# Kernel tuning notes

Hardware: AMD Instinct MI355X
Metric: run time of the kernel (lower is better)

The kernel has to match this reference:

```python
import jax, jax.numpy as jnp
import numpy as np

B, O, H, I = 256, 128, 1024, 2048  # batch, objects, hidden, input_size
Hh = H // 2  # 512; x_j feature dim
DF = I - Hh  # 1536; X_F feature dim


def _xavier(key, shape):
    fan_in, fan_out = shape[1], shape[0]
    lim = np.sqrt(6.0 / (fan_in + fan_out))
    return jax.random.uniform(key, shape, jnp.float32, -lim, lim)


def setup_inputs() -> dict:
    key = jax.random.key(0)
    ks = jax.random.split(key, 24)
    mask = jax.random.bernoulli(ks[0], 0.7, (B, O))
    mask = mask.at[:, 0].set(True)  # ensure at least one valid object per row
    inp = {
        "x_j": jax.random.normal(ks[1], (B, O, Hh), jnp.float32),
        "x_mask": mask,
        "X_F": jax.random.normal(ks[2], (B, DF), jnp.float32),
        "h": jax.random.normal(ks[3], (B, 1, H), jnp.float32),
        "c": jax.random.normal(ks[4], (B, 1, H), jnp.float32),
    }
    names_W = ["W_i", "W_f", "W_c", "W_o"]
    names_U = ["U_i", "U_f", "U_c", "U_o"]
    names_V = ["V_i", "V_f", "V_c", "V_o"]
    k = 5
    for n in names_W:
        inp[n] = _xavier(ks[k], (H, I)); k += 1
    for n in names_U + names_V:
        inp[n] = _xavier(ks[k], (H, H)); k += 1
    for n in ["b_i", "b_f", "b_c", "b_o"]:
        inp[n] = jnp.zeros((H,), jnp.float32)
    inp["w"] = _xavier(ks[k], (1, Hh)); k += 1
    inp["W_e"] = _xavier(ks[k], (Hh, H)); k += 1
    inp["U_e"] = _xavier(ks[k], (Hh, Hh)); k += 1
    inp["b_e"] = jnp.zeros((Hh,), jnp.float32)
    return inp


def reference(x_j, x_mask, X_F, h, c,
              W_i, W_f, W_c, W_o,
              U_i, U_f, U_c, U_o,
              V_i, V_f, V_c, V_o,
              b_i, b_f, b_c, b_o,
              w, W_e, U_e, b_e):
    # Additive attention over objects.
    # h: (B,1,H) -> (B,1,Hh) broadcasts against x_j proj (B,O,Hh)
    e = jnp.tanh(h @ W_e.T + x_j @ U_e.T + b_e)      # (B,O,Hh)
    e = (e @ w.T)[..., 0]                              # (B,O)
    e = jnp.where(x_mask, e, -1e9)
    a = jax.nn.softmax(e, axis=1)                      # (B,O)
    phi_j = jnp.einsum('bo,bok->bk', a, x_j)[:, None, :]  # (B,1,Hh)
    x = jnp.concatenate([phi_j, X_F[:, None, :]], axis=2)  # (B,1,I)

    # Peephole LSTM gates (h, c: (B,1,H))
    i = jax.nn.sigmoid(x @ W_i.T + h @ U_i.T + c @ V_i.T + b_i)
    f = jax.nn.sigmoid(x @ W_f.T + h @ U_f.T + c @ V_f.T + b_f)
    new_c = f * c + i * jnp.tanh(x @ W_c.T + h @ U_c.T + b_c)
    o = jax.nn.sigmoid(x @ W_o.T + h @ U_o.T + c @ V_o.T + b_o)
    new_h = o * jnp.tanh(new_c)
    return new_h, new_c
```

## Files before the change

kernel.cpp:

```cpp
#include <hip/hip_runtime.h>
#include <hip/hip_bf16.h>

typedef unsigned char u8;
typedef unsigned short u16;
typedef unsigned int u32;
typedef __attribute__((ext_vector_type(8))) short bf8;
typedef __attribute__((ext_vector_type(4))) float f4;

#define B_ 256
#define O_ 128
#define Hh_ 512
#define H_ 1024
#define DF_ 1536
#define I_ 2048

#define HWE_OFF   0
#define XC_OFF    524288
#define PRE_OFF   2621440
#define FLAG_OFF  6815744
#define XJ16_OFF  7340032
#define UE16_OFF  40894464
#define WS_BIG    41418752
#define GPART_OFF XJ16_OFF

__device__ __forceinline__ float bf1(u16 u){ union{u32 i; float f;} v; v.i = ((u32)u)<<16; return v.f; }
__device__ __forceinline__ u16 f2bf(float f){
    __hip_bfloat16 h = __float2bfloat16(f);
    union{ __hip_bfloat16 h; u16 u; } v; v.h = h; return v.u;
}
__device__ __forceinline__ u32 pack2(float a, float b){
    return ((u32)f2bf(a)) | (((u32)f2bf(b))<<16);
}
struct P8 { uint4 lo, hi; };
__device__ __forceinline__ P8 fetch8(const void* p, size_t idx, int isf32){
    P8 r;
    if(isf32){
        const uint4* f = (const uint4*)((const float*)p + idx);
        r.lo = f[0]; r.hi = f[1];
    } else {
        r.lo = *(const uint4*)((const u16*)p + idx);
    }
    return r;
}
__device__ __forceinline__ uint4 cvt8(P8 r, int isf32){
    if(isf32){
        float4 x = *(float4*)&r.lo, y = *(float4*)&r.hi;
        uint4 o;
        o.x = pack2(x.x,x.y); o.y = pack2(x.z,x.w);
        o.z = pack2(y.x,y.y); o.w = pack2(y.z,y.w);
        return o;
    }
    return r.lo;
}
__device__ __forceinline__ uint4 load8(const void* p, size_t idx, int isf32){
    return cvt8(fetch8(p, idx, isf32), isf32);
}
__device__ __forceinline__ float loads(const void* p, size_t idx, int isf32){
    return isf32 ? ((const float*)p)[idx] : bf1(((const u16*)p)[idx]);
}
__device__ __forceinline__ float fast_tanh(float x){
    return 1.0f - 2.0f/(__expf(2.0f*x)+1.0f);
}
__device__ __forceinline__ float sigmoidf_(float x){
    return 1.0f/(1.0f+__expf(-x));
}

__global__ void k_detect(const u8* __restrict__ m, const u16* __restrict__ xj,
                         int* __restrict__ flags){
    __shared__ int n1, n2, n3, mb, xo;
    int t = threadIdx.x;
    if(t==0){ n1=0; n2=0; n3=0; mb=0; xo=0; }
    __syncthreads();
    int a1=0, a2=0, a3=0, amax=0;
    for(int i=t; i<8192; i+=256){
        int v = m[i]; int c = i&3;
        if(c==1) a1|=v;
        if(c==2) a2|=v;
        if(c==3) a3|=v;
        amax = amax > v ? amax : v;
    }
    if(a1) atomicOr(&n1,1);
    if(a2) atomicOr(&n2,1);
    if(a3) atomicOr(&n3,1);
    atomicMax(&mb, amax);
    int e = 0;
    for(int i=t; i<2048; i+=256){
        u32 u = xj[2*i];
        int ex = (u>>7)&0xFF;
        if(ex >= 156) e = 1;
    }
    if(e) atomicOr(&xo,1);
    __syncthreads();
    if(t==0){
        int w;
        if(!n1 && !n2 && !n3)      w = 4;
        else if(!n1 && n2 && n3)   w = 4;
        else if(mb > 1)            w = 2;
        else                       w = 1;
        flags[0] = w;
        flags[1] = xo;
    }
}

__global__ __launch_bounds__(256) void k_pack(const void* __restrict__ XF,
                                              const void* __restrict__ h,
                                              const void* __restrict__ c,
                                              const void* __restrict__ Ue,
                                              const int* __restrict__ flags,
                                              int packN,
                                              u16* __restrict__ Xc,
                                              u16* __restrict__ ue16){
    int bid = blockIdx.x, t = threadIdx.x;
    int isf32 = flags[1];
    if(bid < packN){
        int b = bid/14;
        int r = (bid%14)*256 + t;
        float v;
        if(r < DF_)            v = loads(XF, (size_t)b*DF_ + r, isf32);
        else if(r < DF_ + H_)  v = loads(h,  (size_t)b*H_ + (r - DF_), isf32);
        else                   v = loads(c,  (size_t)b*H_ + (r - DF_ - H_), isf32);
        Xc[(size_t)b*4096 + 512 + r] = f2bf(v);
    } else {
        size_t g = (size_t)(bid - packN)*256 + t;
        size_t idx = g*8;
        *(uint4*)&ue16[idx] = load8(Ue, idx, isf32);
    }
}

__global__ __launch_bounds__(256) void k_hwe(const void* __restrict__ h,
                                             const void* __restrict__ We,
                                             const int* __restrict__ flags,
                                             float* __restrict__ hwe){
    int n0 = blockIdx.x*64;
    int kc = blockIdx.y*128;
    int m0 = blockIdx.z*128;
    int t = threadIdx.x;
    int isf32 = flags[1];
    __shared__ __align__(16) u16 As[128*40];
    __shared__ __align__(16) u16 Bs[64*40];
    int w = t>>6, lane = t&63;
    int q = lane>>4, l16 = lane&15;
    int koff = q*8;
    f4 acc[2][4];
    for(int mi=0;mi<2;mi++) for(int ni=0;ni<4;ni++){
        f4 z = {0.f,0.f,0.f,0.f}; acc[mi][ni] = z;
    }
    for(int ks=0; ks<128; ks+=32){
        __syncthreads();
        for(int i=0;i<2;i++){
            int row = i*64 + (t>>2), cv = t&3;
            uint4 va = load8(h, (size_t)(m0+row)*H_ + kc + ks + cv*8, isf32);
            *(uint4*)&As[row*40 + cv*8] = va;
        }
        {
            int row = t>>2, cv = t&3;
            uint4 vb = load8(We, (size_t)(n0+row)*H_ + kc + ks + cv*8, isf32);
            *(uint4*)&Bs[row*40 + cv*8] = vb;
        }
        __syncthreads();
        bf8 af[2], bfr[4];
        for(int mi=0;mi<2;mi++) af[mi]  = *(const bf8*)&As[(w*32+mi*16+l16)*40 + koff];
        for(int ni=0;ni<4;ni++) bfr[ni] = *(const bf8*)&Bs[(ni*16+l16)*40 + koff];
        for(int mi=0;mi<2;mi++)
            for(int ni=0;ni<4;ni++)
                acc[mi][ni] = __builtin_amdgcn_mfma_f32_16x16x32_bf16(af[mi], bfr[ni], acc[mi][ni], 0,0,0);
    }
    for(int mi=0;mi<2;mi++){
        for(int r=0;r<4;r++){
            int brow = m0 + w*32 + mi*16 + q*4 + r;
            for(int ni=0;ni<4;ni++){
                int ncol = n0 + ni*16 + l16;
                atomicAdd(&hwe[(size_t)brow*Hh_ + ncol], acc[mi][ni][r]);
            }
        }
    }
}

__global__ __launch_bounds__(512) void k_attn(const void* __restrict__ xjA,
                                              const void* __restrict__ wvec,
                                              const void* __restrict__ UeA,
                                              const void* __restrict__ be,
                                              const float* __restrict__ hwe,
                                              const int* __restrict__ flags,
                                              int srcbfB,
                                              float* __restrict__ Epart){
    int b = blockIdx.x, y = blockIdx.y, t = threadIdx.x;
    int isf = flags[1];
    int isA = isf;
    int isB = srcbfB ? 0 : isf;
    __shared__ __align__(16) u16 As[128*40];
    __shared__ __align__(16) u16 Bs[128*40];
    __shared__ float hwes[128];
    __shared__ float wvs[128];

    if(t < 128){
        int col = y*128 + t;
        hwes[t] = hwe[(size_t)b*Hh_ + col] + loads(be, col, isf);
        wvs[t]  = loads(wvec, col, isf);
    }

    const size_t xboff = (size_t)b*O_*Hh_;
    int w = t>>6, lane = t&63;
    int q = lane>>4, l16 = lane&15;
    int koff = q*8;
    int rA = t>>2, cA = t&3;

    f4 acc[8];
    for(int ni=0;ni<8;ni++){
        f4 z = {0.f,0.f,0.f,0.f}; acc[ni] = z;
    }

    P8 pa, pb;
    pa = fetch8(xjA, xboff + (size_t)rA*Hh_        + cA*8, isA);
    pb = fetch8(UeA, (size_t)(y*128 + rA)*Hh_      + cA*8, isB);

    for(int ks=0; ks<Hh_; ks+=32){
        __syncthreads();
        *(uint4*)&As[rA*40 + cA*8] = cvt8(pa, isA);
        *(uint4*)&Bs[rA*40 + cA*8] = cvt8(pb, isB);
        __syncthreads();
        if(ks + 32 < Hh_){
            int kn = ks + 32;
            pa = fetch8(xjA, xboff + (size_t)rA*Hh_        + kn + cA*8, isA);
            pb = fetch8(UeA, (size_t)(y*128 + rA)*Hh_      + kn + cA*8, isB);
        }
        bf8 af, bfr[8];
        af = *(const bf8*)&As[(w*16+l16)*40 + koff];
        for(int ni=0;ni<8;ni++) bfr[ni] = *(const bf8*)&Bs[(ni*16+l16)*40 + koff];
        for(int ni=0;ni<8;ni++)
            acc[ni] = __builtin_amdgcn_mfma_f32_16x16x32_bf16(af, bfr[ni], acc[ni], 0,0,0);
    }
    for(int r=0;r<4;r++){
        int o = w*16 + q*4 + r;
        float part = 0.f;
        for(int ni=0;ni<8;ni++){
            int col = ni*16 + l16;
            part += wvs[col] * fast_tanh(hwes[col] + acc[ni][r]);
        }
        part += __shfl_xor(part, 1);
        part += __shfl_xor(part, 2);
        part += __shfl_xor(part, 4);
        part += __shfl_xor(part, 8);
        if(l16 == 0) Epart[(size_t)y*32768 + (size_t)b*O_ + o] = part;
    }
}

__global__ __launch_bounds__(512) void k_soft(const float* __restrict__ Epart,
                                              const void* __restrict__ maskp,
                                              const void* __restrict__ xjA,
                                              const int* __restrict__ flags,
                                              u16* __restrict__ Xc){
    int b = blockIdx.x, t = threadIdx.x;
    int isf = flags[1];
    int isA = isf;
    int mw = flags[0];
    __shared__ float es[O_];
    __shared__ float as_[O_];
    __shared__ float red[2];
    if(t < O_){
        float e = 0.f;
        for(int p=0;p<4;p++) e += Epart[(size_t)p*32768 + (size_t)b*O_ + t];
        size_t mi_ = (size_t)b*O_ + t;
        bool valid;
        if(mw == 1)      valid = ((const u8*)maskp)[mi_]  != 0;
        else if(mw == 2) valid = ((const u16*)maskp)[mi_] != 0;
        else             valid = ((const u32*)maskp)[mi_] != 0;
        es[t] = valid ? e : -1e30f;
    }
    __syncthreads();
    if(t < 64){
        float v = fmaxf(es[t], es[t+64]);
        for(int m=32;m>0;m>>=1) v = fmaxf(v, __shfl_xor(v, m));
        if(t==0) red[0] = v;
    }
    __syncthreads();
    if(t < O_) as_[t] = __expf(es[t] - red[0]);
    __syncthreads();
    if(t < 64){
        float v = as_[t] + as_[t+64];
        for(int m=32;m>0;m>>=1) v += __shfl_xor(v, m);
        if(t==0) red[1] = v;
    }
    __syncthreads();
    float inv = 1.0f / red[1];
    float acc = 0.f;
    size_t base = (size_t)b*O_*Hh_ + t;
    #pragma unroll 8
    for(int o=0;o<O_;o++){
        acc += as_[o] * loads(xjA, base + (size_t)o*Hh_, isA);
    }
    Xc[(size_t)b*4096 + t] = f2bf(acc * inv);
}

__global__ __launch_bounds__(512) void k_gates(const u16* __restrict__ Xc,
    const void* __restrict__ Wi, const void* __restrict__ Wf, const void* __restrict__ Wc, const void* __restrict__ Wo,
    const void* __restrict__ Ui, const void* __restrict__ Uf, const void* __restrict__ Uc, const void* __restrict__ Uo,
    const void* __restrict__ Vi, const void* __restrict__ Vf, const void* __restrict__ Vo,
    const int* __restrict__ flags,
    int dosplit,
    float* __restrict__ part){
    int nt = blockIdx.x;
    int kc = blockIdx.y;
    int g  = nt>>4;
    int k0 = kc*512;
    if(g == 2 && k0 >= 3072) return;
    int isf32 = flags[1];
    const void* Wm = (g==0)?Wi:(g==1)?Wf:(g==2)?Wc:Wo;
    const void* Um = (g==0)?Ui:(g==1)?Uf:(g==2)?Uc:Uo;
    const void* Vm = (g==0)?Vi:(g==1)?Vf:(g==3)?Vo:Vi;
    int n0 = (nt&15)*64;
    int t = threadIdx.x;
    __shared__ __align__(16) u16 As[256*40];
    __shared__ __align__(16) u16 Bs[64*40];
    int w = t>>6, lane = t&63;
    int q = lane>>4, l16 = lane&15;
    int koff = q*8;
    int rA = t>>2, cA = t&3;
    bool hasB = (t < 256);

    f4 acc[2][4];
    for(int mi=0;mi<2;mi++) for(int ni=0;ni<4;ni++){
        f4 z = {0.f,0.f,0.f,0.f}; acc[mi][ni] = z;
    }

    auto fetchB = [&](int k)->P8{
        int n = n0 + rA;
        if(k < 2048)       return fetch8(Wm, (size_t)n*I_ + k, isf32);
        else if(k < 3072)  return fetch8(Um, (size_t)n*H_ + (k-2048), isf32);
        else               return fetch8(Vm, (size_t)n*H_ + (k-3072), isf32);
    };

    uint4 qa0, qa1; P8 qb;
    qa0 = *(const uint4*)(Xc + (size_t)rA*4096       + k0 + cA*8);
    qa1 = *(const uint4*)(Xc + (size_t)(rA+128)*4096 + k0 + cA*8);
    if(hasB) qb = fetchB(k0 + cA*8);

    for(int ks=0; ks<512; ks+=32){
        __syncthreads();
        *(uint4*)&As[rA*40 + cA*8]       = qa0;
        *(uint4*)&As[(rA+128)*40 + cA*8] = qa1;
        if(hasB) *(uint4*)&Bs[rA*40 + cA*8] = cvt8(qb, isf32);
        __syncthreads();
        if(ks + 32 < 512){
            int kn = k0 + ks + 32;
            qa0 = *(const uint4*)(Xc + (size_t)rA*4096       + kn + cA*8);
            qa1 = *(const uint4*)(Xc + (size_t)(rA+128)*4096 + kn + cA*8);
            if(hasB) qb = fetchB(kn + cA*8);
        }
        bf8 af[2], bfr[4];
        for(int mi=0;mi<2;mi++) af[mi]  = *(const bf8*)&As[(w*32+mi*16+l16)*40 + koff];
        for(int ni=0;ni<4;ni++) bfr[ni] = *(const bf8*)&Bs[(ni*16+l16)*40 + koff];
        for(int mi=0;mi<2;mi++)
            for(int ni=0;ni<4;ni++)
                acc[mi][ni] = __builtin_amdgcn_mfma_f32_16x16x32_bf16(af[mi], bfr[ni], acc[mi][ni], 0,0,0);
    }
    float* pg = dosplit ? (part + ((size_t)kc*4 + g)*(size_t)(B_*H_))
                        : (part + (size_t)g*(B_*H_));
    for(int mi=0;mi<2;mi++){
        for(int r=0;r<4;r++){
            int brow = w*32 + mi*16 + q*4 + r;
            for(int ni=0;ni<4;ni++){
                int ncol = n0 + ni*16 + l16;
                size_t o = (size_t)brow*H_ + ncol;
                if(dosplit) pg[o] = acc[mi][ni][r];
                else        atomicAdd(&pg[o], acc[mi][ni][r]);
            }
        }
    }
}

__global__ __launch_bounds__(256) void k_combine(const float* __restrict__ part,
    int nsplit, int climit,
    const void* __restrict__ c,
    const void* __restrict__ bi, const void* __restrict__ bfv,
    const void* __restrict__ bc, const void* __restrict__ bo,
    const int* __restrict__ flags,
    float* __restrict__ out){
    int b = blockIdx.x, t = threadIdx.x;
    int isf32 = flags[1];
    const size_t G = (size_t)B_*H_;
    for(int i=0;i<4;i++){
        int n = i*256 + t;
        size_t idx = (size_t)b*H_ + n;
        float pi = 0.f, pf = 0.f, pcv = 0.f, po = 0.f;
        for(int p=0;p<nsplit;p++){
            const float* pp = part + (size_t)p*4*G;
            pi += pp[idx];
            pf += pp[G + idx];
            po += pp[3*G + idx];
            if(p < climit) pcv += pp[2*G + idx];
        }
        pi  += loads(bi,  n, isf32);
        pf  += loads(bfv, n, isf32);
        pcv += loads(bc,  n, isf32);
        po  += loads(bo,  n, isf32);
        float ig = sigmoidf_(pi);
        float fg = sigmoidf_(pf);
        float og = sigmoidf_(po);
        float cold = loads(c, idx, isf32);
        float ncv = fg*cold + ig*fast_tanh(pcv);
        float nh  = og*fast_tanh(ncv);
        out[idx]     = nh;
        out[G + idx] = ncv;
    }
}

extern "C" void kernel_launch(void* const* d_in, const int* in_sizes, int n_in,
                              void* d_out, int out_size, void* d_ws, size_t ws_size,
                              hipStream_t stream){
    const void* xj   = d_in[0];
    const void* mask = d_in[1];
    const void* XF   = d_in[2];
    const void* h    = d_in[3];
    const void* c    = d_in[4];
    const void* Wi   = d_in[5];
    const void* Wf   = d_in[6];
    const void* Wc   = d_in[7];
    const void* Wo   = d_in[8];
    const void* Ui   = d_in[9];
    const void* Uf   = d_in[10];
    const void* Uc   = d_in[11];
    const void* Uo   = d_in[12];
    const void* Vi   = d_in[13];
    const void* Vf   = d_in[14];
    const void* Vo   = d_in[16];
    const void* bi   = d_in[17];
    const void* bfv  = d_in[18];
    const void* bc   = d_in[19];
    const void* bo   = d_in[20];
    const void* wv   = d_in[21];
    const void* We   = d_in[22];
    const void* Ue   = d_in[23];
    const void* be   = d_in[24];

    char* ws = (char*)d_ws;
    float* hwe  = (float*)(ws + HWE_OFF);
    u16*   Xc   = (u16*)(ws + XC_OFF);
    float* pre  = (float*)(ws + PRE_OFF);
    int*   flags= (int*)(ws + FLAG_OFF);
    float* out  = (float*)d_out;

    int big = (ws_size >= (size_t)WS_BIG);
    u16* ue16 = (u16*)(ws + UE16_OFF);
    float* gpart = (float*)(ws + GPART_OFF);
    const void* UeA = big ? (const void*)ue16 : Ue;

    k_detect<<<1, 256, 0, stream>>>((const u8*)mask, (const u16*)xj, flags);
    hipMemsetAsync(hwe, 0, (size_t)B_*Hh_*sizeof(float), stream);
    k_pack<<<3584 + (big ? 256 : 0), 256, 0, stream>>>(XF, h, c, Ue, flags, 3584, Xc, ue16);
    k_hwe<<<dim3(8,8,2), 256, 0, stream>>>(h, We, flags, hwe);
    k_attn<<<dim3(B_, 4), 512, 0, stream>>>(xj, wv, UeA, be, hwe, flags, big, pre);
    k_soft<<<B_, 512, 0, stream>>>(pre, mask, xj, flags, Xc);
    if(big){
        k_gates<<<dim3(64, 8), 512, 0, stream>>>(Xc, Wi,Wf,Wc,Wo, Ui,Uf,Uc,Uo, Vi,Vf,Vo, flags, 1, gpart);
        k_combine<<<B_, 256, 0, stream>>>(gpart, 8, 6, c, bi, bfv, bc, bo, flags, out);
    } else {
        hipMemsetAsync(pre, 0, (size_t)4*B_*H_*sizeof(float), stream);
        k_gates<<<dim3(64, 8), 512, 0, stream>>>(Xc, Wi,Wf,Wc,Wo, Ui,Uf,Uc,Uo, Vi,Vf,Vo, flags, 0, pre);
        k_combine<<<B_, 256, 0, stream>>>(pre, 1, 1, c, bi, bfv, bc, bo, flags, out);
    }
}
```

Baseline: 297.7 us.

## Fuse detect, pack and hwe GEMM into one prep kernel and drop memset

Removes the single-block detect kernel and its flags buffer; each kernel now works out the dtype and mask-width flags itself with a wave ballot on a few elements. The Ue conversion, the h·We^T GEMM and the X packing are merged into one launch, and the hwe memset plus atomics are replaced by four split-K partial buffers that k_attn sums. This cuts three launches and the serial detect step, at the cost of redundant detection reads in every block and a heuristic that samples fewer elements. hweP sits inside the PRE region, which the attention partials also use, so overlap is a risk.

```diff
diff --git a/kernel.cpp b/kernel.cpp
--- a/kernel.cpp
+++ b/kernel.cpp
@@ -14,10 +14,9 @@
 #define DF_ 1536
 #define I_ 2048
 
-#define HWE_OFF   0
 #define XC_OFF    524288
 #define PRE_OFF   2621440
-#define FLAG_OFF  6815744
+#define HWEP_OFF  (PRE_OFF + 1048576)
 #define XJ16_OFF  7340032
 #define UE16_OFF  40894464
 #define WS_BIG    41418752
@@ -65,54 +64,99 @@
     return 1.0f/(1.0f+__expf(-x));
 }
 
-__global__ void k_detect(const u8* __restrict__ m, const u16* __restrict__ xj,
-                         int* __restrict__ flags){
-    __shared__ int n1, n2, n3, mb, xo;
-    int t = threadIdx.x;
-    if(t==0){ n1=0; n2=0; n3=0; mb=0; xo=0; }
-    __syncthreads();
-    int a1=0, a2=0, a3=0, amax=0;
-    for(int i=t; i<8192; i+=256){
-        int v = m[i]; int c = i&3;
-        if(c==1) a1|=v;
-        if(c==2) a2|=v;
-        if(c==3) a3|=v;
-        amax = amax > v ? amax : v;
-    }
-    if(a1) atomicOr(&n1,1);
-    if(a2) atomicOr(&n2,1);
-    if(a3) atomicOr(&n3,1);
-    atomicMax(&mb, amax);
-    int e = 0;
-    for(int i=t; i<2048; i+=256){
-        u32 u = xj[2*i];
-        int ex = (u>>7)&0xFF;
-        if(ex >= 156) e = 1;
-    }
-    if(e) atomicOr(&xo,1);
-    __syncthreads();
-    if(t==0){
-        int w;
-        if(!n1 && !n2 && !n3)      w = 4;
-        else if(!n1 && n2 && n3)   w = 4;
-        else if(mb > 1)            w = 2;
-        else                       w = 1;
-        flags[0] = w;
-        flags[1] = xo;
-    }
-}
-
-__global__ __launch_bounds__(256) void k_pack(const void* __restrict__ XF,
+__device__ __forceinline__ int detect_isf32(const void* xj){
+    int l = threadIdx.x & 63;
+    u32 u = ((const u16*)xj)[2*l];
+    int ex = (u>>7)&0xFF;
+    unsigned long long m = __ballot(ex >= 156);
+    return m != 0ULL;
+}
+__device__ __forceinline__ int detect_mw(const void* maskp){
+    int l = threadIdx.x & 63;
+    u32 v = ((const u32*)maskp)[l];
+    int b0 =  v      & 0xFF;
+    int b1 = (v>>8)  & 0xFF;
+    int b2 = (v>>16) & 0xFF;
+    int b3 = (v>>24) & 0xFF;
+    unsigned long long n1 = __ballot(b1 != 0);
+    unsigned long long n2 = __ballot(b2 != 0);
+    unsigned long long n3 = __ballot(b3 != 0);
+    int mx = max(max(b0,b1), max(b2,b3));
+    for(int s=32;s>0;s>>=1) mx = max(mx, __shfl_xor(mx, s));
+    int w;
+    if(!n1 && !n2 && !n3)      w = 4;
+    else if(!n1 && n2 && n3)   w = 4;
+    else if(mx > 1)            w = 2;
+    else                       w = 1;
+    return w;
+}
+
+__global__ __launch_bounds__(256) void k_prep(const void* __restrict__ xj,
+                                              const void* __restrict__ Ue,
+                                              const void* __restrict__ XF,
                                               const void* __restrict__ h,
                                               const void* __restrict__ c,
-                                              const void* __restrict__ Ue,
-                                              const int* __restrict__ flags,
-                                              int packN,
-                                              u16* __restrict__ Xc,
-                                              u16* __restrict__ ue16){
+                                              const void* __restrict__ We,
+                                              int ueN,
+                                              u16* __restrict__ ue16,
+                                              float* __restrict__ hweP,
+                                              u16* __restrict__ Xc){
     int bid = blockIdx.x, t = threadIdx.x;
-    int isf32 = flags[1];
-    if(bid < packN){
+    int isf32 = detect_isf32(xj);
+    if(bid < ueN){
+        size_t g = (size_t)bid*256 + t;
+        size_t idx = g*8;
+        *(uint4*)&ue16[idx] = load8(Ue, idx, isf32);
+        return;
+    }
+    bid -= ueN;
+    if(bid < 64){
+        int n0 = (bid&7)*64;
+        int kb = ((bid>>3)&3)*256;
+        int m0 = (bid>>5)*128;
+        __shared__ __align__(16) u16 As[128*40];
+        __shared__ __align__(16) u16 Bs[64*40];
+        int w = t>>6, lane = t&63;
+        int q = lane>>4, l16 = lane&15;
+        int koff = q*8;
+        f4 acc[2][4];
+        for(int mi=0;mi<2;mi++) for(int ni=0;ni<4;ni++){
+            f4 z = {0.f,0.f,0.f,0.f}; acc[mi][ni] = z;
+        }
+        for(int ks=0; ks<256; ks+=32){
+            __syncthreads();
+            for(int i=0;i<2;i++){
+                int row = i*64 + (t>>2), cv = t&3;
+                uint4 va = load8(h, (size_t)(m0+row)*H_ + kb + ks + cv*8, isf32);
+                *(uint4*)&As[row*40 + cv*8] = va;
+            }
+            {
+                int row = t>>2, cv = t&3;
+                uint4 vb = load8(We, (size_t)(n0+row)*H_ + kb + ks + cv*8, isf32);
+                *(uint4*)&Bs[row*40 + cv*8] = vb;
+            }
+            __syncthreads();
+            bf8 af[2], bfr[4];
+            for(int mi=0;mi<2;mi++) af[mi]  = *(const bf8*)&As[(w*32+mi*16+l16)*40 + koff];
+            for(int ni=0;ni<4;ni++) bfr[ni] = *(const bf8*)&Bs[(ni*16+l16)*40 + koff];
+            for(int mi=0;mi<2;mi++)
+                for(int ni=0;ni<4;ni++)
+                    acc[mi][ni] = __builtin_amdgcn_mfma_f32_16x16x32_bf16(af[mi], bfr[ni], acc[mi][ni], 0,0,0);
+        }
+        float* hp = hweP + (size_t)((bid>>3)&3)*(B_*Hh_);
+        for(int mi=0;mi<2;mi++){
+            for(int r=0;r<4;r++){
+                int brow = m0 + w*32 + mi*16 + q*4 + r;
+                for(int ni=0;ni<4;ni++){
+                    int ncol = n0 + ni*16 + l16;
+                    hp[(size_t)brow*Hh_ + ncol] = acc[mi][ni][r];
+                }
+            }
+        }
+        return;
+    }
+    bid -= 64;
+    {
         int b = bid/14;
         int r = (bid%14)*256 + t;
         float v;
@@ -120,59 +164,6 @@
         else if(r < DF_ + H_)  v = loads(h,  (size_t)b*H_ + (r - DF_), isf32);
         else                   v = loads(c,  (size_t)b*H_ + (r - DF_ - H_), isf32);
         Xc[(size_t)b*4096 + 512 + r] = f2bf(v);
-    } else {
-        size_t g = (size_t)(bid - packN)*256 + t;
-        size_t idx = g*8;
-        *(uint4*)&ue16[idx] = load8(Ue, idx, isf32);
-    }
-}
-
-__global__ __launch_bounds__(256) void k_hwe(const void* __restrict__ h,
-                                             const void* __restrict__ We,
-                                             const int* __restrict__ flags,
-                                             float* __restrict__ hwe){
-    int n0 = blockIdx.x*64;
-    int kc = blockIdx.y*128;
-    int m0 = blockIdx.z*128;
-    int t = threadIdx.x;
-    int isf32 = flags[1];
-    __shared__ __align__(16) u16 As[128*40];
-    __shared__ __align__(16) u16 Bs[64*40];
-    int w = t>>6, lane = t&63;
-    int q = lane>>4, l16 = lane&15;
-    int koff = q*8;
-    f4 acc[2][4];
-    for(int mi=0;mi<2;mi++) for(int ni=0;ni<4;ni++){
-        f4 z = {0.f,0.f,0.f,0.f}; acc[mi][ni] = z;
-    }
-    for(int ks=0; ks<128; ks+=32){
-        __syncthreads();
-        for(int i=0;i<2;i++){
-            int row = i*64 + (t>>2), cv = t&3;
-            uint4 va = load8(h, (size_t)(m0+row)*H_ + kc + ks + cv*8, isf32);
-            *(uint4*)&As[row*40 + cv*8] = va;
-        }
-        {
-            int row = t>>2, cv = t&3;
-            uint4 vb = load8(We, (size_t)(n0+row)*H_ + kc + ks + cv*8, isf32);
-            *(uint4*)&Bs[row*40 + cv*8] = vb;
-        }
-        __syncthreads();
-        bf8 af[2], bfr[4];
-        for(int mi=0;mi<2;mi++) af[mi]  = *(const bf8*)&As[(w*32+mi*16+l16)*40 + koff];
-        for(int ni=0;ni<4;ni++) bfr[ni] = *(const bf8*)&Bs[(ni*16+l16)*40 + koff];
-        for(int mi=0;mi<2;mi++)
-            for(int ni=0;ni<4;ni++)
-                acc[mi][ni] = __builtin_amdgcn_mfma_f32_16x16x32_bf16(af[mi], bfr[ni], acc[mi][ni], 0,0,0);
-    }
-    for(int mi=0;mi<2;mi++){
-        for(int r=0;r<4;r++){
-            int brow = m0 + w*32 + mi*16 + q*4 + r;
-            for(int ni=0;ni<4;ni++){
-                int ncol = n0 + ni*16 + l16;
-                atomicAdd(&hwe[(size_t)brow*Hh_ + ncol], acc[mi][ni][r]);
-            }
-        }
     }
 }
 
@@ -180,12 +171,11 @@
                                               const void* __restrict__ wvec,
                                               const void* __restrict__ UeA,
                                               const void* __restrict__ be,
-                                              const float* __restrict__ hwe,
-                                              const int* __restrict__ flags,
+                                              const float* __restrict__ hweP,
                                               int srcbfB,
                                               float* __restrict__ Epart){
     int b = blockIdx.x, y = blockIdx.y, t = threadIdx.x;
-    int isf = flags[1];
+    int isf = detect_isf32(xjA);
     int isA = isf;
     int isB = srcbfB ? 0 : isf;
     __shared__ __align__(16) u16 As[128*40];
@@ -195,7 +185,10 @@
 
     if(t < 128){
         int col = y*128 + t;
-        hwes[t] = hwe[(size_t)b*Hh_ + col] + loads(be, col, isf);
+        float s = 0.f;
+        #pragma unroll
+        for(int p=0;p<4;p++) s += hweP[(size_t)p*(B_*Hh_) + (size_t)b*Hh_ + col];
+        hwes[t] = s + loads(be, col, isf);
         wvs[t]  = loads(wvec, col, isf);
     }
 
@@ -248,12 +241,11 @@
 __global__ __launch_bounds__(512) void k_soft(const float* __restrict__ Epart,
                                               const void* __restrict__ maskp,
                                               const void* __restrict__ xjA,
-                                              const int* __restrict__ flags,
                                               u16* __restrict__ Xc){
     int b = blockIdx.x, t = threadIdx.x;
-    int isf = flags[1];
+    int isf = detect_isf32(xjA);
     int isA = isf;
-    int mw = flags[0];
+    int mw = detect_mw(maskp);
     __shared__ float es[O_];
     __shared__ float as_[O_];
     __shared__ float red[2];
@@ -293,10 +285,10 @@
 }
 
 __global__ __launch_bounds__(512) void k_gates(const u16* __restrict__ Xc,
+    const void* __restrict__ xjdet,
     const void* __restrict__ Wi, const void* __restrict__ Wf, const void* __restrict__ Wc, const void* __restrict__ Wo,
     const void* __restrict__ Ui, const void* __restrict__ Uf, const void* __restrict__ Uc, const void* __restrict__ Uo,
     const void* __restrict__ Vi, const void* __restrict__ Vf, const void* __restrict__ Vo,
-    const int* __restrict__ flags,
     int dosplit,
     float* __restrict__ part){
     int nt = blockIdx.x;
@@ -304,7 +296,7 @@
     int g  = nt>>4;
     int k0 = kc*512;
     if(g == 2 && k0 >= 3072) return;
-    int isf32 = flags[1];
+    int isf32 = detect_isf32(xjdet);
     const void* Wm = (g==0)?Wi:(g==1)?Wf:(g==2)?Wc:Wo;
     const void* Um = (g==0)?Ui:(g==1)?Uf:(g==2)?Uc:Uo;
     const void* Vm = (g==0)?Vi:(g==1)?Vf:(g==3)?Vo:Vi;
@@ -371,13 +363,13 @@
 
 __global__ __launch_bounds__(256) void k_combine(const float* __restrict__ part,
     int nsplit, int climit,
+    const void* __restrict__ xjdet,
     const void* __restrict__ c,
     const void* __restrict__ bi, const void* __restrict__ bfv,
     const void* __restrict__ bc, const void* __restrict__ bo,
-    const int* __restrict__ flags,
     float* __restrict__ out){
     int b = blockIdx.x, t = threadIdx.x;
-    int isf32 = flags[1];
+    int isf32 = detect_isf32(xjdet);
     const size_t G = (size_t)B_*H_;
     for(int i=0;i<4;i++){
         int n = i*256 + t;
@@ -434,29 +426,27 @@
     const void* be   = d_in[24];
 
     char* ws = (char*)d_ws;
-    float* hwe  = (float*)(ws + HWE_OFF);
-    u16*   Xc   = (u16*)(ws + XC_OFF);
-    float* pre  = (float*)(ws + PRE_OFF);
-    int*   flags= (int*)(ws + FLAG_OFF);
-    float* out  = (float*)d_out;
+    u16*   Xc    = (u16*)(ws + XC_OFF);
+    float* Epart = (float*)(ws + PRE_OFF);
+    float* hweP  = (float*)(ws + HWEP_OFF);
+    float* pre   = (float*)(ws + PRE_OFF);
+    float* out   = (float*)d_out;
 
     int big = (ws_size >= (size_t)WS_BIG);
     u16* ue16 = (u16*)(ws + UE16_OFF);
     float* gpart = (float*)(ws + GPART_OFF);
     const void* UeA = big ? (const void*)ue16 : Ue;
 
-    k_detect<<<1, 256, 0, stream>>>((const u8*)mask, (const u16*)xj, flags);
-    hipMemsetAsync(hwe, 0, (size_t)B_*Hh_*sizeof(float), stream);
-    k_pack<<<3584 + (big ? 256 : 0), 256, 0, stream>>>(XF, h, c, Ue, flags, 3584, Xc, ue16);
-    k_hwe<<<dim3(8,8,2), 256, 0, stream>>>(h, We, flags, hwe);
-    k_attn<<<dim3(B_, 4), 512, 0, stream>>>(xj, wv, UeA, be, hwe, flags, big, pre);
-    k_soft<<<B_, 512, 0, stream>>>(pre, mask, xj, flags, Xc);
+    int ueN = big ? 256 : 0;
+    k_prep<<<ueN + 64 + 3584, 256, 0, stream>>>(xj, Ue, XF, h, c, We, ueN, ue16, hweP, Xc);
+    k_attn<<<dim3(B_, 4), 512, 0, stream>>>(xj, wv, UeA, be, hweP, big, Epart);
+    k_soft<<<B_, 512, 0, stream>>>(Epart, mask, xj, Xc);
     if(big){
-        k_gates<<<dim3(64, 8), 512, 0, stream>>>(Xc, Wi,Wf,Wc,Wo, Ui,Uf,Uc,Uo, Vi,Vf,Vo, flags, 1, gpart);
-        k_combine<<<B_, 256, 0, stream>>>(gpart, 8, 6, c, bi, bfv, bc, bo, flags, out);
+        k_gates<<<dim3(64, 8), 512, 0, stream>>>(Xc, xj, Wi,Wf,Wc,Wo, Ui,Uf,Uc,Uo, Vi,Vf,Vo, 1, gpart);
+        k_combine<<<B_, 256, 0, stream>>>(gpart, 8, 6, xj, c, bi, bfv, bc, bo, out);
     } else {
         hipMemsetAsync(pre, 0, (size_t)4*B_*H_*sizeof(float), stream);
-        k_gates<<<dim3(64, 8), 512, 0, stream>>>(Xc, Wi,Wf,Wc,Wo, Ui,Uf,Uc,Uo, Vi,Vf,Vo, flags, 0, pre);
-        k_combine<<<B_, 256, 0, stream>>>(pre, 1, 1, c, bi, bfv, bc, bo, flags, out);
-    }
-}
+        k_gates<<<dim3(64, 8), 512, 0, stream>>>(Xc, xj, Wi,Wf,Wc,Wo, Ui,Uf,Uc,Uo, Vi,Vf,Vo, 0, pre);
+        k_combine<<<B_, 256, 0, stream>>>(pre, 1, 1, xj, c, bi, bfv, bc, bo, out);
+    }
+}
```

New measurement: 283.7 us. 1.05x faster.
